# Optimization experiments

Hardware: AMD Instinct MI355X
Metric: run time of the kernel (lower is better)

## Reference

```python
import jax, jax.numpy as jnp
import numpy as np

B, S, D = 4096, 64, 256
EPS = 1e-12

def setup_inputs() -> dict:
    key = jax.random.key(0)
    k1, k2 = jax.random.split(key)
    x = jax.random.normal(k1, (B, S, D), dtype=jnp.float32)
    complex_weight = jax.random.normal(k2, (1, S // 2 + 1, D, 2), dtype=jnp.float32)
    gamma = jnp.ones((D,), dtype=jnp.float32)
    beta = jnp.zeros((D,), dtype=jnp.float32)
    return {"x": x, "complex_weight": complex_weight, "gamma": gamma, "beta": beta}

def reference(x, complex_weight, gamma, beta):
    # x: [B, S, D]; complex_weight: [1, S//2+1, D, 2]
    w = jax.lax.complex(complex_weight[..., 0], complex_weight[..., 1])  # [1, F, D]
    xf = jnp.fft.rfft(x, axis=1, norm='ortho')          # [B, F, D] complex
    y = jnp.fft.irfft(xf * w, n=x.shape[1], axis=1, norm='ortho')  # [B, S, D]
    # dropout is identity (p=0 / eval); residual + LayerNorm (eps=1e-12)
    h = y + x
    mu = jnp.mean(h, axis=-1, keepdims=True)
    var = jnp.mean(jnp.square(h - mu), axis=-1, keepdims=True)
    return (h - mu) * jax.lax.rsqrt(var + EPS) * gamma + beta
```

## Files before the change

### kernel.cpp

```cpp
#include <hip/hip_runtime.h>
#include <math.h>


typedef __attribute__((ext_vector_type(8))) short short8;
typedef __attribute__((ext_vector_type(4))) float f32x4;
typedef __attribute__((ext_vector_type(4))) unsigned int u32x4;
typedef __attribute__((ext_vector_type(2))) unsigned int u32x2;

#define VROW 144

__device__ __forceinline__ unsigned short bf16rn(float v) {
    unsigned u = __float_as_uint(v);
    u += 0x7fffu + ((u >> 16) & 1u);
    return (unsigned short)(u >> 16);
}
__device__ __forceinline__ unsigned cvtpk(float a, float b) {
    unsigned r;
    asm("v_cvt_pk_bf16_f32 %0, %1, %2" : "=v"(r) : "v"(a), "v"(b));
    return r;
}

__global__ void pack_A_kernel(unsigned short* __restrict__ apack) {
    const int bid  = blockIdx.x;
    const int lane = threadIdx.x;
    const float step = 6.28318530717958647692f / 64.f;
    const int fid = bid & 7;
    const int kt = fid >> 2, mi = fid & 3;
    const int m = mi * 16 + (lane & 15);
    if (bid < 8) {
        unsigned short* dst = apack + ((size_t)fid * 64 + lane) * 8;
        #pragma unroll
        for (int j = 0; j < 8; ++j) {
            const int t = kt * 32 + 8 * (lane >> 4) + j;
            float val;
            if (m <= 32) val =  cosf(step * (float)((m * t) & 63)) * 0.125f;
            else         val = -sinf(step * (float)(((m - 32) * t) & 63)) * 0.125f;
            dst[j] = bf16rn(val);
        }
    } else {
        unsigned short* dst = apack + 4096 + ((size_t)fid * 64 + lane) * 8;
        #pragma unroll
        for (int j = 0; j < 8; ++j) {
            const int c = kt * 32 + 8 * (lane >> 4) + j;
            float val;
            if (c == 0)       val = 0.125f;
            else if (c == 32) val = (m & 1) ? -0.125f : 0.125f;
            else if (c < 32)  val =  0.25f * cosf(step * (float)((c * m) & 63));
            else              val = -0.25f * sinf(step * (float)(((c - 32) * m) & 63));
            dst[j] = bf16rn(val);
        }
    }
}

#define MFMA(A, B, C) __builtin_amdgcn_mfma_f32_16x16x32_bf16( \
    __builtin_bit_cast(short8, A), (B), (C), 0, 0, 0)

__global__ __launch_bounds__(256, 4)
void fft_ln_kernel(const float* __restrict__ x,
                   const float* __restrict__ cw,
                   const float* __restrict__ gamma,
                   const float* __restrict__ beta,
                   const unsigned short* __restrict__ apack,
                   float* __restrict__ out) {
    __shared__ __align__(16) char smem[4 * 64 * VROW];
    __shared__ float mr[128];
    const int tid = threadIdx.x, lane = tid & 63, wv = tid >> 6;
    const int hi = lane >> 4, lm = lane & 15;
    const int b = blockIdx.x, dbase = wv * 64;
    const float* __restrict__ xb = x + (size_t)b * 16384;
    const u32x4* __restrict__ ap1 = (const u32x4*)apack;
    const u32x4* __restrict__ ap2 = (const u32x4*)(apack + 4096);

    f32x4 acc[16];
    #pragma unroll
    for (int i = 0; i < 16; ++i) acc[i] = (f32x4)0.f;

    #pragma unroll
    for (int kt = 0; kt < 2; ++kt) {
        const u32x4 af0 = ap1[(kt * 4 + 0) * 64 + lane];
        const u32x4 af1 = ap1[(kt * 4 + 1) * 64 + lane];
        const u32x4 af2 = ap1[(kt * 4 + 2) * 64 + lane];
        const u32x4 af3 = ap1[(kt * 4 + 3) * 64 + lane];
        const float* __restrict__ xp = xb + (kt * 32 + 8 * hi) * 256 + dbase + lm;
        #pragma unroll
        for (int ni = 0; ni < 4; ++ni) {
            float xv[8];
            #pragma unroll
            for (int j = 0; j < 8; ++j) xv[j] = xp[j * 256 + ni * 16];
            u32x4 bw;
            bw[0] = cvtpk(xv[0], xv[1]);
            bw[1] = cvtpk(xv[2], xv[3]);
            bw[2] = cvtpk(xv[4], xv[5]);
            bw[3] = cvtpk(xv[6], xv[7]);
            const short8 bb = __builtin_bit_cast(short8, bw);
            acc[0 * 4 + ni] = MFMA(af0, bb, acc[0 * 4 + ni]);
            acc[1 * 4 + ni] = MFMA(af1, bb, acc[1 * 4 + ni]);
            acc[2 * 4 + ni] = MFMA(af2, bb, acc[2 * 4 + ni]);
            acc[3 * 4 + ni] = MFMA(af3, bb, acc[3 * 4 + ni]);
        }
    }

    #pragma unroll
    for (int mi = 0; mi < 2; ++mi)
    #pragma unroll
    for (int ni = 0; ni < 4; ++ni) {
        const int d = dbase + ni * 16 + lm;
        #pragma unroll
        for (int r = 0; r < 4; ++r) {
            const int f = mi * 16 + hi * 4 + r;
            const float2 wc = *(const float2*)(cw + ((size_t)(f * 256 + d)) * 2);
            const float wr1 = wc.x + 1.f;
            const float Ure = acc[mi * 4 + ni][r];
            const float Uim = acc[(mi + 2) * 4 + ni][r];
            float Vre = Ure * wr1 - Uim * wc.y;
            float Vim = Ure * wc.y + Uim * wr1;
            if (mi == 0 && r == 0) {
                const float w32 = cw[(32 * 256 + d) * 2] + 1.f;
                if (hi == 0) { Vre = Ure * wr1; Vim = Uim * w32; }
            }
            acc[mi * 4 + ni][r]       = Vre;
            acc[(mi + 2) * 4 + ni][r] = Vim;
        }
    }

    char* vb = smem + wv * 64 * VROW;
    #pragma unroll
    for (int mi = 0; mi < 4; ++mi)
    #pragma unroll
    for (int ni = 0; ni < 4; ++ni) {
        const f32x4 a4 = acc[mi * 4 + ni];
        u32x2 p;
        p[0] = cvtpk(a4[0], a4[1]);
        p[1] = cvtpk(a4[2], a4[3]);
        const int dl = ni * 16 + lm;
        *(u32x2*)(vb + dl * VROW + mi * 32 + hi * 8) = p;
    }

    #pragma unroll
    for (int i = 0; i < 16; ++i) acc[i] = (f32x4)0.f;
    #pragma unroll
    for (int kt = 0; kt < 2; ++kt) {
        const u32x4 af0 = ap2[(kt * 4 + 0) * 64 + lane];
        const u32x4 af1 = ap2[(kt * 4 + 1) * 64 + lane];
        const u32x4 af2 = ap2[(kt * 4 + 2) * 64 + lane];
        const u32x4 af3 = ap2[(kt * 4 + 3) * 64 + lane];
        #pragma unroll
        for (int ni = 0; ni < 4; ++ni) {
            const int dl = ni * 16 + lm;
            const u32x4 bw = *(const u32x4*)(vb + dl * VROW + kt * 64 + hi * 16);
            const short8 bb = __builtin_bit_cast(short8, bw);
            acc[0 * 4 + ni] = MFMA(af0, bb, acc[0 * 4 + ni]);
            acc[1 * 4 + ni] = MFMA(af1, bb, acc[1 * 4 + ni]);
            acc[2 * 4 + ni] = MFMA(af2, bb, acc[2 * 4 + ni]);
            acc[3 * 4 + ni] = MFMA(af3, bb, acc[3 * 4 + ni]);
        }
    }

    __syncthreads();
    float* psum = (float*)smem;
    float* psq  = (float*)smem + 64 * 66;
    #pragma unroll
    for (int mi = 0; mi < 4; ++mi)
    #pragma unroll
    for (int r = 0; r < 4; ++r) {
        float s1 = 0.f, s2 = 0.f;
        #pragma unroll
        for (int ni = 0; ni < 4; ++ni) {
            const float v = acc[mi * 4 + ni][r];
            s1 += v;
            s2 = fmaf(v, v, s2);
        }
        const int row = mi * 16 + hi * 4 + r;
        psum[row * 66 + wv * 16 + lm] = s1;
        psq [row * 66 + wv * 16 + lm] = s2;
    }
    __syncthreads();
    if (tid < 64) {
        float s1 = 0.f, s2 = 0.f;
        #pragma unroll
        for (int j = 0; j < 64; ++j) {
            s1 += psum[tid * 66 + j];
            s2 += psq [tid * 66 + j];
        }
        const float mean = s1 * (1.f / 256.f);
        const float var  = s2 * (1.f / 256.f) - mean * mean;
        mr[tid * 2 + 0] = mean;
        mr[tid * 2 + 1] = rsqrtf(var + 1e-12f);
    }
    __syncthreads();

    f32x4 gv, bv;
    #pragma unroll
    for (int ni = 0; ni < 4; ++ni) {
        gv[ni] = gamma[dbase + ni * 16 + lm];
        bv[ni] = beta [dbase + ni * 16 + lm];
    }
    float* __restrict__ ob = out + (size_t)b * 16384;
    #pragma unroll
    for (int mi = 0; mi < 4; ++mi)
    #pragma unroll
    for (int r = 0; r < 4; ++r) {
        const int row = mi * 16 + hi * 4 + r;
        const float m  = mr[row * 2 + 0];
        const float rs = mr[row * 2 + 1];
        #pragma unroll
        for (int ni = 0; ni < 4; ++ni)
            ob[row * 256 + dbase + ni * 16 + lm] =
                (acc[mi * 4 + ni][r] - m) * rs * gv[ni] + bv[ni];
    }
}

extern "C" void kernel_launch(void* const* d_in, const int* in_sizes, int n_in,
                              void* d_out, int out_size, void* d_ws, size_t ws_size,
                              hipStream_t stream) {
    const float* x     = (const float*)d_in[0];
    const float* cw    = (const float*)d_in[1];
    const float* gamma = (const float*)d_in[2];
    const float* beta  = (const float*)d_in[3];
    float* outp = (float*)d_out;
    unsigned short* apack = (unsigned short*)d_ws;

    pack_A_kernel<<<16, 64, 0, stream>>>(apack);
    fft_ln_kernel<<<4096, 256, 0, stream>>>(x, cw, gamma, beta, apack, outp);
}
```

Measured before the change: 130.0 us.

## Vectorize x and weight loads with lane-to-column remap, parallelize LayerNorm reduction

Each lane now owns four adjacent feature columns. That lets the input rows and the complex weights be fetched as 16-byte vector loads instead of scalar or float2 loads. The shared-memory staging index is remapped so the second MFMA still reads columns in their original order. The per-row LayerNorm sum is now a two-stage reduction across all four waves instead of one wave doing a 64-element serial loop. The cost is one extra barrier and a few more live registers for the vector loads.

```diff
diff --git a/kernel.cpp b/kernel.cpp
--- a/kernel.cpp
+++ b/kernel.cpp
@@ -81,17 +81,18 @@
         const u32x4 af1 = ap1[(kt * 4 + 1) * 64 + lane];
         const u32x4 af2 = ap1[(kt * 4 + 2) * 64 + lane];
         const u32x4 af3 = ap1[(kt * 4 + 3) * 64 + lane];
-        const float* __restrict__ xp = xb + (kt * 32 + 8 * hi) * 256 + dbase + lm;
-        #pragma unroll
-        for (int ni = 0; ni < 4; ++ni) {
-            float xv[8];
-            #pragma unroll
-            for (int j = 0; j < 8; ++j) xv[j] = xp[j * 256 + ni * 16];
+        const float* __restrict__ xp = xb + (kt * 32 + 8 * hi) * 256 + dbase + 4 * lm;
+        f32x4 xq[8];
+        #pragma unroll
+        for (int j = 0; j < 8; ++j)
+            xq[j] = *(const f32x4*)(xp + j * 256);
+        #pragma unroll
+        for (int ni = 0; ni < 4; ++ni) {
             u32x4 bw;
-            bw[0] = cvtpk(xv[0], xv[1]);
-            bw[1] = cvtpk(xv[2], xv[3]);
-            bw[2] = cvtpk(xv[4], xv[5]);
-            bw[3] = cvtpk(xv[6], xv[7]);
+            bw[0] = cvtpk(xq[0][ni], xq[1][ni]);
+            bw[1] = cvtpk(xq[2][ni], xq[3][ni]);
+            bw[2] = cvtpk(xq[4][ni], xq[5][ni]);
+            bw[3] = cvtpk(xq[6][ni], xq[7][ni]);
             const short8 bb = __builtin_bit_cast(short8, bw);
             acc[0 * 4 + ni] = MFMA(af0, bb, acc[0 * 4 + ni]);
             acc[1 * 4 + ni] = MFMA(af1, bb, acc[1 * 4 + ni]);
@@ -100,23 +101,30 @@
         }
     }
 
+    const float* __restrict__ cwb = cw + 2 * (size_t)(dbase + 4 * lm);
+    f32x4 nqa = *(const f32x4*)(cwb + 2 * 32 * 256);
+    f32x4 nqb = *(const f32x4*)(cwb + 2 * 32 * 256 + 4);
+    float w32r[4] = {nqa[0], nqa[2], nqb[0], nqb[2]};
     #pragma unroll
     for (int mi = 0; mi < 2; ++mi)
     #pragma unroll
-    for (int ni = 0; ni < 4; ++ni) {
-        const int d = dbase + ni * 16 + lm;
-        #pragma unroll
-        for (int r = 0; r < 4; ++r) {
-            const int f = mi * 16 + hi * 4 + r;
-            const float2 wc = *(const float2*)(cw + ((size_t)(f * 256 + d)) * 2);
-            const float wr1 = wc.x + 1.f;
+    for (int r = 0; r < 4; ++r) {
+        const int f = mi * 16 + hi * 4 + r;
+        const f32x4 ca = *(const f32x4*)(cwb + 2 * (size_t)f * 256);
+        const f32x4 cb = *(const f32x4*)(cwb + 2 * (size_t)f * 256 + 4);
+        #pragma unroll
+        for (int ni = 0; ni < 4; ++ni) {
+            const float wre = (ni == 0) ? ca[0] : (ni == 1) ? ca[2]
+                            : (ni == 2) ? cb[0] : cb[2];
+            const float wim = (ni == 0) ? ca[1] : (ni == 1) ? ca[3]
+                            : (ni == 2) ? cb[1] : cb[3];
+            const float wr1 = wre + 1.f;
             const float Ure = acc[mi * 4 + ni][r];
             const float Uim = acc[(mi + 2) * 4 + ni][r];
-            float Vre = Ure * wr1 - Uim * wc.y;
-            float Vim = Ure * wc.y + Uim * wr1;
+            float Vre = Ure * wr1 - Uim * wim;
+            float Vim = Ure * wim + Uim * wr1;
             if (mi == 0 && r == 0) {
-                const float w32 = cw[(32 * 256 + d) * 2] + 1.f;
-                if (hi == 0) { Vre = Ure * wr1; Vim = Uim * w32; }
+                if (hi == 0) { Vre = Ure * wr1; Vim = Uim * (w32r[ni] + 1.f); }
             }
             acc[mi * 4 + ni][r]       = Vre;
             acc[(mi + 2) * 4 + ni][r] = Vim;
@@ -132,7 +140,7 @@
         u32x2 p;
         p[0] = cvtpk(a4[0], a4[1]);
         p[1] = cvtpk(a4[2], a4[3]);
-        const int dl = ni * 16 + lm;
+        const int dl = 4 * lm + ni;
         *(u32x2*)(vb + dl * VROW + mi * 32 + hi * 8) = p;
     }
 
@@ -159,6 +167,8 @@
     __syncthreads();
     float* psum = (float*)smem;
     float* psq  = (float*)smem + 64 * 66;
+    float* ps2  = (float*)smem + 2 * 64 * 66;
+    float* pq2  = (float*)smem + 2 * 64 * 66 + 320;
     #pragma unroll
     for (int mi = 0; mi < 4; ++mi)
     #pragma unroll
@@ -175,13 +185,21 @@
         psq [row * 66 + wv * 16 + lm] = s2;
     }
     __syncthreads();
+    {
+        const int row = tid & 63;
+        float s1 = 0.f, s2 = 0.f;
+        #pragma unroll
+        for (int j = 0; j < 16; ++j) {
+            s1 += psum[row * 66 + wv * 16 + j];
+            s2 += psq [row * 66 + wv * 16 + j];
+        }
+        ps2[row * 5 + wv] = s1;
+        pq2[row * 5 + wv] = s2;
+    }
+    __syncthreads();
     if (tid < 64) {
-        float s1 = 0.f, s2 = 0.f;
-        #pragma unroll
-        for (int j = 0; j < 64; ++j) {
-            s1 += psum[tid * 66 + j];
-            s2 += psq [tid * 66 + j];
-        }
+        const float s1 = ps2[tid * 5] + ps2[tid * 5 + 1] + ps2[tid * 5 + 2] + ps2[tid * 5 + 3];
+        const float s2 = pq2[tid * 5] + pq2[tid * 5 + 1] + pq2[tid * 5 + 2] + pq2[tid * 5 + 3];
         const float mean = s1 * (1.f / 256.f);
         const float var  = s2 * (1.f / 256.f) - mean * mean;
         mr[tid * 2 + 0] = mean;
```

Result: slower. 146.8 us (+12.9%).

## Swizzle LDS staging, parallelize LN reduction with packed bf16 partials, raise occupancy

Applied to the files above, without the earlier changes.

Shrinks the spectral staging row stride to 128 bytes with an XOR swizzle to avoid bank conflicts, and caps shared memory at 32KB so five blocks fit per CU under the new launch bound. The LayerNorm row reduction becomes a two-stage reduce spread across all threads instead of 64 threads looping over 64 entries. Partial sums are packed as bf16 pairs to halve LDS traffic. The bf16 rounding of sums and sums of squares risks accuracy loss in the variance.

```diff
diff --git a/kernel.cpp b/kernel.cpp
--- a/kernel.cpp
+++ b/kernel.cpp
@@ -7,12 +7,15 @@
 typedef __attribute__((ext_vector_type(4))) unsigned int u32x4;
 typedef __attribute__((ext_vector_type(2))) unsigned int u32x2;
 
-#define VROW 144
+#define VROW 128
 
 __device__ __forceinline__ unsigned short bf16rn(float v) {
     unsigned u = __float_as_uint(v);
     u += 0x7fffu + ((u >> 16) & 1u);
     return (unsigned short)(u >> 16);
+}
+__device__ __forceinline__ float bf16tof(unsigned short h) {
+    return __uint_as_float(((unsigned)h) << 16);
 }
 __device__ __forceinline__ unsigned cvtpk(float a, float b) {
     unsigned r;
@@ -55,15 +58,14 @@
 #define MFMA(A, B, C) __builtin_amdgcn_mfma_f32_16x16x32_bf16( \
     __builtin_bit_cast(short8, A), (B), (C), 0, 0, 0)
 
-__global__ __launch_bounds__(256, 4)
+__global__ __launch_bounds__(256, 5)
 void fft_ln_kernel(const float* __restrict__ x,
                    const float* __restrict__ cw,
                    const float* __restrict__ gamma,
                    const float* __restrict__ beta,
                    const unsigned short* __restrict__ apack,
                    float* __restrict__ out) {
-    __shared__ __align__(16) char smem[4 * 64 * VROW];
-    __shared__ float mr[128];
+    __shared__ __align__(16) char smem[32768];
     const int tid = threadIdx.x, lane = tid & 63, wv = tid >> 6;
     const int hi = lane >> 4, lm = lane & 15;
     const int b = blockIdx.x, dbase = wv * 64;
@@ -133,7 +135,9 @@
         p[0] = cvtpk(a4[0], a4[1]);
         p[1] = cvtpk(a4[2], a4[3]);
         const int dl = ni * 16 + lm;
-        *(u32x2*)(vb + dl * VROW + mi * 32 + hi * 8) = p;
+        unsigned off = (unsigned)(dl * VROW + mi * 32 + hi * 8);
+        off ^= (unsigned)((dl & 7) << 4);
+        *(u32x2*)(vb + off) = p;
     }
 
     #pragma unroll
@@ -147,7 +151,9 @@
         #pragma unroll
         for (int ni = 0; ni < 4; ++ni) {
             const int dl = ni * 16 + lm;
-            const u32x4 bw = *(const u32x4*)(vb + dl * VROW + kt * 64 + hi * 16);
+            unsigned off = (unsigned)(dl * VROW + kt * 64 + hi * 16);
+            off ^= (unsigned)((dl & 7) << 4);
+            const u32x4 bw = *(const u32x4*)(vb + off);
             const short8 bb = __builtin_bit_cast(short8, bw);
             acc[0 * 4 + ni] = MFMA(af0, bb, acc[0 * 4 + ni]);
             acc[1 * 4 + ni] = MFMA(af1, bb, acc[1 * 4 + ni]);
@@ -157,8 +163,10 @@
     }
 
     __syncthreads();
-    float* psum = (float*)smem;
-    float* psq  = (float*)smem + 64 * 66;
+    unsigned* pp = (unsigned*)smem;
+    float* ps2 = (float*)(smem + 17408);
+    float* pq2 = (float*)(smem + 18688);
+    float* mr  = (float*)(smem + 19968);
     #pragma unroll
     for (int mi = 0; mi < 4; ++mi)
     #pragma unroll
@@ -171,17 +179,25 @@
             s2 = fmaf(v, v, s2);
         }
         const int row = mi * 16 + hi * 4 + r;
-        psum[row * 66 + wv * 16 + lm] = s1;
-        psq [row * 66 + wv * 16 + lm] = s2;
+        pp[row * 68 + wv * 16 + lm] = cvtpk(s1, s2);
+    }
+    __syncthreads();
+    {
+        const int row = tid & 63;
+        float s1 = 0.f, s2 = 0.f;
+        #pragma unroll
+        for (int j = 0; j < 16; ++j) {
+            const unsigned v = pp[row * 68 + wv * 16 + j];
+            s1 += bf16tof((unsigned short)(v & 0xffffu));
+            s2 += bf16tof((unsigned short)(v >> 16));
+        }
+        ps2[row * 5 + wv] = s1;
+        pq2[row * 5 + wv] = s2;
     }
     __syncthreads();
     if (tid < 64) {
-        float s1 = 0.f, s2 = 0.f;
-        #pragma unroll
-        for (int j = 0; j < 64; ++j) {
-            s1 += psum[tid * 66 + j];
-            s2 += psq [tid * 66 + j];
-        }
+        const float s1 = ps2[tid * 5] + ps2[tid * 5 + 1] + ps2[tid * 5 + 2] + ps2[tid * 5 + 3];
+        const float s2 = pq2[tid * 5] + pq2[tid * 5 + 1] + pq2[tid * 5 + 2] + pq2[tid * 5 + 3];
         const float mean = s1 * (1.f / 256.f);
         const float var  = s2 * (1.f / 256.f) - mean * mean;
         mr[tid * 2 + 0] = mean;
```

New measurement: 201.4 us. +55.0%, slower.

## Process four batches per block and parallelize LayerNorm row reduction

Applied to the files above, without the earlier changes.

Each block now loops over four batch elements instead of one, so the grid shrinks to a quarter. The LayerNorm statistics reduction becomes two stages: all four waves first sum 16 partials each, then one wave combines four values, replacing a serial 64-element loop in a single wave. This cuts block-launch overhead and the serial reduction tail, but adds barriers per batch and leaves 1024 blocks, which may under-fill the GPU and removes cross-block latency hiding.

```diff
diff --git a/kernel.cpp b/kernel.cpp
--- a/kernel.cpp
+++ b/kernel.cpp
@@ -55,6 +55,8 @@
 #define MFMA(A, B, C) __builtin_amdgcn_mfma_f32_16x16x32_bf16( \
     __builtin_bit_cast(short8, A), (B), (C), 0, 0, 0)
 
+#define BPB 4
+
 __global__ __launch_bounds__(256, 4)
 void fft_ln_kernel(const float* __restrict__ x,
                    const float* __restrict__ cw,
@@ -63,150 +65,165 @@
                    const unsigned short* __restrict__ apack,
                    float* __restrict__ out) {
     __shared__ __align__(16) char smem[4 * 64 * VROW];
+    __shared__ float ps2[64 * 5];
+    __shared__ float pq2[64 * 5];
     __shared__ float mr[128];
     const int tid = threadIdx.x, lane = tid & 63, wv = tid >> 6;
     const int hi = lane >> 4, lm = lane & 15;
-    const int b = blockIdx.x, dbase = wv * 64;
-    const float* __restrict__ xb = x + (size_t)b * 16384;
+    const int dbase = wv * 64;
     const u32x4* __restrict__ ap1 = (const u32x4*)apack;
     const u32x4* __restrict__ ap2 = (const u32x4*)(apack + 4096);
 
-    f32x4 acc[16];
-    #pragma unroll
-    for (int i = 0; i < 16; ++i) acc[i] = (f32x4)0.f;
-
-    #pragma unroll
-    for (int kt = 0; kt < 2; ++kt) {
-        const u32x4 af0 = ap1[(kt * 4 + 0) * 64 + lane];
-        const u32x4 af1 = ap1[(kt * 4 + 1) * 64 + lane];
-        const u32x4 af2 = ap1[(kt * 4 + 2) * 64 + lane];
-        const u32x4 af3 = ap1[(kt * 4 + 3) * 64 + lane];
-        const float* __restrict__ xp = xb + (kt * 32 + 8 * hi) * 256 + dbase + lm;
+    #pragma unroll 1
+    for (int bb = 0; bb < BPB; ++bb) {
+        const int b = blockIdx.x * BPB + bb;
+        const float* __restrict__ xb = x + (size_t)b * 16384;
+
+        f32x4 acc[16];
+        #pragma unroll
+        for (int i = 0; i < 16; ++i) acc[i] = (f32x4)0.f;
+
+        #pragma unroll
+        for (int kt = 0; kt < 2; ++kt) {
+            const u32x4 af0 = ap1[(kt * 4 + 0) * 64 + lane];
+            const u32x4 af1 = ap1[(kt * 4 + 1) * 64 + lane];
+            const u32x4 af2 = ap1[(kt * 4 + 2) * 64 + lane];
+            const u32x4 af3 = ap1[(kt * 4 + 3) * 64 + lane];
+            const float* __restrict__ xp = xb + (kt * 32 + 8 * hi) * 256 + dbase + lm;
+            #pragma unroll
+            for (int ni = 0; ni < 4; ++ni) {
+                float xv[8];
+                #pragma unroll
+                for (int j = 0; j < 8; ++j) xv[j] = xp[j * 256 + ni * 16];
+                u32x4 bw;
+                bw[0] = cvtpk(xv[0], xv[1]);
+                bw[1] = cvtpk(xv[2], xv[3]);
+                bw[2] = cvtpk(xv[4], xv[5]);
+                bw[3] = cvtpk(xv[6], xv[7]);
+                const short8 bbv = __builtin_bit_cast(short8, bw);
+                acc[0 * 4 + ni] = MFMA(af0, bbv, acc[0 * 4 + ni]);
+                acc[1 * 4 + ni] = MFMA(af1, bbv, acc[1 * 4 + ni]);
+                acc[2 * 4 + ni] = MFMA(af2, bbv, acc[2 * 4 + ni]);
+                acc[3 * 4 + ni] = MFMA(af3, bbv, acc[3 * 4 + ni]);
+            }
+        }
+
+        #pragma unroll
+        for (int mi = 0; mi < 2; ++mi)
         #pragma unroll
         for (int ni = 0; ni < 4; ++ni) {
-            float xv[8];
-            #pragma unroll
-            for (int j = 0; j < 8; ++j) xv[j] = xp[j * 256 + ni * 16];
-            u32x4 bw;
-            bw[0] = cvtpk(xv[0], xv[1]);
-            bw[1] = cvtpk(xv[2], xv[3]);
-            bw[2] = cvtpk(xv[4], xv[5]);
-            bw[3] = cvtpk(xv[6], xv[7]);
-            const short8 bb = __builtin_bit_cast(short8, bw);
-            acc[0 * 4 + ni] = MFMA(af0, bb, acc[0 * 4 + ni]);
-            acc[1 * 4 + ni] = MFMA(af1, bb, acc[1 * 4 + ni]);
-            acc[2 * 4 + ni] = MFMA(af2, bb, acc[2 * 4 + ni]);
-            acc[3 * 4 + ni] = MFMA(af3, bb, acc[3 * 4 + ni]);
-        }
-    }
-
-    #pragma unroll
-    for (int mi = 0; mi < 2; ++mi)
-    #pragma unroll
-    for (int ni = 0; ni < 4; ++ni) {
-        const int d = dbase + ni * 16 + lm;
+            const int d = dbase + ni * 16 + lm;
+            #pragma unroll
+            for (int r = 0; r < 4; ++r) {
+                const int f = mi * 16 + hi * 4 + r;
+                const float2 wc = *(const float2*)(cw + ((size_t)(f * 256 + d)) * 2);
+                const float wr1 = wc.x + 1.f;
+                const float Ure = acc[mi * 4 + ni][r];
+                const float Uim = acc[(mi + 2) * 4 + ni][r];
+                float Vre = Ure * wr1 - Uim * wc.y;
+                float Vim = Ure * wc.y + Uim * wr1;
+                if (mi == 0 && r == 0) {
+                    const float w32 = cw[(32 * 256 + d) * 2] + 1.f;
+                    if (hi == 0) { Vre = Ure * wr1; Vim = Uim * w32; }
+                }
+                acc[mi * 4 + ni][r]       = Vre;
+                acc[(mi + 2) * 4 + ni][r] = Vim;
+            }
+        }
+
+        char* vb = smem + wv * 64 * VROW;
+        #pragma unroll
+        for (int mi = 0; mi < 4; ++mi)
+        #pragma unroll
+        for (int ni = 0; ni < 4; ++ni) {
+            const f32x4 a4 = acc[mi * 4 + ni];
+            u32x2 p;
+            p[0] = cvtpk(a4[0], a4[1]);
+            p[1] = cvtpk(a4[2], a4[3]);
+            const int dl = ni * 16 + lm;
+            *(u32x2*)(vb + dl * VROW + mi * 32 + hi * 8) = p;
+        }
+
+        #pragma unroll
+        for (int i = 0; i < 16; ++i) acc[i] = (f32x4)0.f;
+        #pragma unroll
+        for (int kt = 0; kt < 2; ++kt) {
+            const u32x4 af0 = ap2[(kt * 4 + 0) * 64 + lane];
+            const u32x4 af1 = ap2[(kt * 4 + 1) * 64 + lane];
+            const u32x4 af2 = ap2[(kt * 4 + 2) * 64 + lane];
+            const u32x4 af3 = ap2[(kt * 4 + 3) * 64 + lane];
+            #pragma unroll
+            for (int ni = 0; ni < 4; ++ni) {
+                const int dl = ni * 16 + lm;
+                const u32x4 bw = *(const u32x4*)(vb + dl * VROW + kt * 64 + hi * 16);
+                const short8 bbv = __builtin_bit_cast(short8, bw);
+                acc[0 * 4 + ni] = MFMA(af0, bbv, acc[0 * 4 + ni]);
+                acc[1 * 4 + ni] = MFMA(af1, bbv, acc[1 * 4 + ni]);
+                acc[2 * 4 + ni] = MFMA(af2, bbv, acc[2 * 4 + ni]);
+                acc[3 * 4 + ni] = MFMA(af3, bbv, acc[3 * 4 + ni]);
+            }
+        }
+
+        __syncthreads();
+        float* psum = (float*)smem;
+        float* psq  = (float*)smem + 64 * 66;
+        #pragma unroll
+        for (int mi = 0; mi < 4; ++mi)
         #pragma unroll
         for (int r = 0; r < 4; ++r) {
-            const int f = mi * 16 + hi * 4 + r;
-            const float2 wc = *(const float2*)(cw + ((size_t)(f * 256 + d)) * 2);
-            const float wr1 = wc.x + 1.f;
-            const float Ure = acc[mi * 4 + ni][r];
-            const float Uim = acc[(mi + 2) * 4 + ni][r];
-            float Vre = Ure * wr1 - Uim * wc.y;
-            float Vim = Ure * wc.y + Uim * wr1;
-            if (mi == 0 && r == 0) {
-                const float w32 = cw[(32 * 256 + d) * 2] + 1.f;
-                if (hi == 0) { Vre = Ure * wr1; Vim = Uim * w32; }
-            }
-            acc[mi * 4 + ni][r]       = Vre;
-            acc[(mi + 2) * 4 + ni][r] = Vim;
-        }
-    }
-
-    char* vb = smem + wv * 64 * VROW;
-    #pragma unroll
-    for (int mi = 0; mi < 4; ++mi)
-    #pragma unroll
-    for (int ni = 0; ni < 4; ++ni) {
-        const f32x4 a4 = acc[mi * 4 + ni];
-        u32x2 p;
-        p[0] = cvtpk(a4[0], a4[1]);
-        p[1] = cvtpk(a4[2], a4[3]);
-        const int dl = ni * 16 + lm;
-        *(u32x2*)(vb + dl * VROW + mi * 32 + hi * 8) = p;
-    }
-
-    #pragma unroll
-    for (int i = 0; i < 16; ++i) acc[i] = (f32x4)0.f;
-    #pragma unroll
-    for (int kt = 0; kt < 2; ++kt) {
-        const u32x4 af0 = ap2[(kt * 4 + 0) * 64 + lane];
-        const u32x4 af1 = ap2[(kt * 4 + 1) * 64 + lane];
-        const u32x4 af2 = ap2[(kt * 4 + 2) * 64 + lane];
-        const u32x4 af3 = ap2[(kt * 4 + 3) * 64 + lane];
+            float s1 = 0.f, s2 = 0.f;
+            #pragma unroll
+            for (int ni = 0; ni < 4; ++ni) {
+                const float v = acc[mi * 4 + ni][r];
+                s1 += v;
+                s2 = fmaf(v, v, s2);
+            }
+            const int row = mi * 16 + hi * 4 + r;
+            psum[row * 66 + wv * 16 + lm] = s1;
+            psq [row * 66 + wv * 16 + lm] = s2;
+        }
+        __syncthreads();
+        {
+            const int row = tid & 63;
+            float s1 = 0.f, s2 = 0.f;
+            #pragma unroll
+            for (int j = 0; j < 16; ++j) {
+                s1 += psum[row * 66 + wv * 16 + j];
+                s2 += psq [row * 66 + wv * 16 + j];
+            }
+            ps2[row * 5 + wv] = s1;
+            pq2[row * 5 + wv] = s2;
+        }
+        __syncthreads();
+        if (tid < 64) {
+            const float s1 = ps2[tid * 5] + ps2[tid * 5 + 1] + ps2[tid * 5 + 2] + ps2[tid * 5 + 3];
+            const float s2 = pq2[tid * 5] + pq2[tid * 5 + 1] + pq2[tid * 5 + 2] + pq2[tid * 5 + 3];
+            const float mean = s1 * (1.f / 256.f);
+            const float var  = s2 * (1.f / 256.f) - mean * mean;
+            mr[tid * 2 + 0] = mean;
+            mr[tid * 2 + 1] = rsqrtf(var + 1e-12f);
+        }
+        __syncthreads();
+
+        f32x4 gv, bv;
         #pragma unroll
         for (int ni = 0; ni < 4; ++ni) {
-            const int dl = ni * 16 + lm;
-            const u32x4 bw = *(const u32x4*)(vb + dl * VROW + kt * 64 + hi * 16);
-            const short8 bb = __builtin_bit_cast(short8, bw);
-            acc[0 * 4 + ni] = MFMA(af0, bb, acc[0 * 4 + ni]);
-            acc[1 * 4 + ni] = MFMA(af1, bb, acc[1 * 4 + ni]);
-            acc[2 * 4 + ni] = MFMA(af2, bb, acc[2 * 4 + ni]);
-            acc[3 * 4 + ni] = MFMA(af3, bb, acc[3 * 4 + ni]);
-        }
-    }
-
-    __syncthreads();
-    float* psum = (float*)smem;
-    float* psq  = (float*)smem + 64 * 66;
-    #pragma unroll
-    for (int mi = 0; mi < 4; ++mi)
-    #pragma unroll
-    for (int r = 0; r < 4; ++r) {
-        float s1 = 0.f, s2 = 0.f;
-        #pragma unroll
-        for (int ni = 0; ni < 4; ++ni) {
-            const float v = acc[mi * 4 + ni][r];
-            s1 += v;
-            s2 = fmaf(v, v, s2);
-        }
-        const int row = mi * 16 + hi * 4 + r;
-        psum[row * 66 + wv * 16 + lm] = s1;
-        psq [row * 66 + wv * 16 + lm] = s2;
-    }
-    __syncthreads();
-    if (tid < 64) {
-        float s1 = 0.f, s2 = 0.f;
-        #pragma unroll
-        for (int j = 0; j < 64; ++j) {
-            s1 += psum[tid * 66 + j];
-            s2 += psq [tid * 66 + j];
-        }
-        const float mean = s1 * (1.f / 256.f);
-        const float var  = s2 * (1.f / 256.f) - mean * mean;
-        mr[tid * 2 + 0] = mean;
-        mr[tid * 2 + 1] = rsqrtf(var + 1e-12f);
-    }
-    __syncthreads();
-
-    f32x4 gv, bv;
-    #pragma unroll
-    for (int ni = 0; ni < 4; ++ni) {
-        gv[ni] = gamma[dbase + ni * 16 + lm];
-        bv[ni] = beta [dbase + ni * 16 + lm];
-    }
-    float* __restrict__ ob = out + (size_t)b * 16384;
-    #pragma unroll
-    for (int mi = 0; mi < 4; ++mi)
-    #pragma unroll
-    for (int r = 0; r < 4; ++r) {
-        const int row = mi * 16 + hi * 4 + r;
-        const float m  = mr[row * 2 + 0];
-        const float rs = mr[row * 2 + 1];
-        #pragma unroll
-        for (int ni = 0; ni < 4; ++ni)
-            ob[row * 256 + dbase + ni * 16 + lm] =
-                (acc[mi * 4 + ni][r] - m) * rs * gv[ni] + bv[ni];
+            gv[ni] = gamma[dbase + ni * 16 + lm];
+            bv[ni] = beta [dbase + ni * 16 + lm];
+        }
+        float* __restrict__ ob = out + (size_t)b * 16384;
+        #pragma unroll
+        for (int mi = 0; mi < 4; ++mi)
+        #pragma unroll
+        for (int r = 0; r < 4; ++r) {
+            const int row = mi * 16 + hi * 4 + r;
+            const float m  = mr[row * 2 + 0];
+            const float rs = mr[row * 2 + 1];
+            #pragma unroll
+            for (int ni = 0; ni < 4; ++ni)
+                ob[row * 256 + dbase + ni * 16 + lm] =
+                    (acc[mi * 4 + ni][r] - m) * rs * gv[ni] + bv[ni];
+        }
     }
 }
 
@@ -221,5 +238,5 @@
     unsigned short* apack = (unsigned short*)d_ws;
 
     pack_A_kernel<<<16, 64, 0, stream>>>(apack);
-    fft_ln_kernel<<<4096, 256, 0, stream>>>(x, cw, gamma, beta, apack, outp);
-}
+    fft_ln_kernel<<<4096 / BPB, 256, 0, stream>>>(x, cw, gamma, beta, apack, outp);
+}
```

Result: slower. 255.2 us (+96.4%).
